# Kernel optimization log

Measured on AMD Instinct MI355X. Metric: run time of the kernel, lower is better.

## Reference

```python
import jax, jax.numpy as jnp
import numpy as np

WINDOW = 512
OVERLAP = 64
STRIDE = WINDOW - OVERLAP  # 448
HEADS = 12
HEAD_DIM = 3072 // HEADS  # 256
SCALE = 1.0 / np.sqrt(HEAD_DIM)


def setup_inputs() -> dict:
    key = jax.random.key(0)
    ks = jax.random.split(key, 9)
    B, S, H = 1, 8192, 3072
    w = 0.02  # weight init scale
    return {
        "hidden_states": jax.random.normal(ks[0], (B, S, H), jnp.float32),
        "Wq": jax.random.normal(ks[1], (H, H), jnp.float32) * w,
        "bq": jnp.zeros((H,), jnp.float32),
        "Wk": jax.random.normal(ks[2], (H, H), jnp.float32) * w,
        "bk": jnp.zeros((H,), jnp.float32),
        "Wv": jax.random.normal(ks[3], (H, H), jnp.float32) * w,
        "bv": jnp.zeros((H,), jnp.float32),
        "Wo": jax.random.normal(ks[4], (H, H), jnp.float32) * w,
        "bo": jnp.zeros((H,), jnp.float32),
    }


def reference(hidden_states, Wq, bq, Wk, bk, Wv, bv, Wo, bo):
    B, S, H = hidden_states.shape
    n_win = -(-S // STRIDE)  # ceil: windows start at 0, STRIDE, 2*STRIDE, ... < S
    starts = np.arange(n_win) * STRIDE                      # static
    idx = starts[:, None] + np.arange(WINDOW)[None, :]      # [n_win, W]
    valid = jnp.asarray(idx < S)                            # [n_win, W] bool
    idx_c = np.minimum(idx, S - 1)                          # clamp for gather

    # Gather overlapping windows: [B, n_win, W, H] (redundant QKV on overlap, as in original)
    win = hidden_states[:, idx_c]

    def proj(Wm, bm):
        y = jnp.einsum('bnwh,oh->bnwo', win, Wm) + bm
        return y.reshape(B, n_win, WINDOW, HEADS, HEAD_DIM)

    q = proj(Wq, bq)
    k = proj(Wk, bk)
    v = proj(Wv, bv)

    scores = jnp.einsum('bnqhd,bnkhd->bnhqk', q, k) * SCALE  # [B,n_win,heads,W,W]
    # Padded (out-of-range) key positions of the short last window must not attend
    scores = jnp.where(valid[None, :, None, None, :], scores, -1e9)
    attn = jax.nn.softmax(scores, axis=-1)
    ctx = jnp.einsum('bnhqk,bnkhd->bnqhd', attn, v)
    ctx = ctx.reshape(B, n_win, WINDOW, H)
    out_w = jnp.einsum('bnwh,oh->bnwo', ctx, Wo) + bo        # [B,n_win,W,H]

    # zero padded query rows, then overlap-add + average
    out_w = out_w * valid[None, :, :, None].astype(out_w.dtype)
    flat_idx = jnp.asarray(idx_c.reshape(-1))                # [n_win*W]
    output = jnp.zeros((B, S, H), out_w.dtype).at[:, flat_idx].add(
        out_w.reshape(B, -1, H))
    counts = jnp.zeros((S,), out_w.dtype).at[flat_idx].add(
        valid.reshape(-1).astype(out_w.dtype))
    return output / jnp.maximum(counts, 1.0)[None, :, None]
```

## Files before the change

kernel.cpp:

```cpp
#include <hip/hip_runtime.h>
#include <hip/hip_bf16.h>
#include <stdint.h>

#define SEQ   8192
#define HDIM  3072
#define NWIN  19
#define WINL  512
#define STR   448
#define NHEAD 12
#define DHEAD 256
#define QKVN  9216
#define ATTN_SCALE 0.0625f

typedef unsigned short u16;
typedef __bf16 bf16x8 __attribute__((ext_vector_type(8)));
typedef float  f32x4  __attribute__((ext_vector_type(4)));
typedef unsigned short us8 __attribute__((ext_vector_type(8)));

__device__ __forceinline__ u16 f2b(float x) {
  return __builtin_bit_cast(u16, __float2bfloat16(x));
}
__device__ __forceinline__ float b2f(u16 u) {
  return __builtin_bit_cast(float, (unsigned int)(u) << 16);
}
__device__ __forceinline__ void gload_lds16(const void* g, void* l) {
  __builtin_amdgcn_global_load_lds(
      (const __attribute__((address_space(1))) void*)g,
      (__attribute__((address_space(3))) void*)l, 16, 0, 0);
}

__global__ __launch_bounds__(256) void cvt_f32_bf16(const float* __restrict__ src,
                                                    u16* __restrict__ dst, int n8) {
  int i = blockIdx.x * 256 + threadIdx.x;
  if (i >= n8) return;
  const float4* s4 = (const float4*)src;
  float4 a = s4[2 * i], b = s4[2 * i + 1];
  us8 o;
  o[0] = f2b(a.x); o[1] = f2b(a.y); o[2] = f2b(a.z); o[3] = f2b(a.w);
  o[4] = f2b(b.x); o[5] = f2b(b.y); o[6] = f2b(b.z); o[7] = f2b(b.w);
  *((us8*)dst + i) = o;
}

__global__ __launch_bounds__(256) void biascat(const float* __restrict__ bq,
                                               const float* __restrict__ bk,
                                               const float* __restrict__ bv,
                                               float* __restrict__ dst) {
  int i = blockIdx.x * 256 + threadIdx.x;
  if (i >= QKVN) return;
  dst[i] = (i < HDIM) ? bq[i] : ((i < 2 * HDIM) ? bk[i - HDIM] : bv[i - 2 * HDIM]);
}

template <bool BF16OUT>
__global__ __launch_bounds__(512, 2) void gemm256(const u16* __restrict__ A,
                                                  const u16* __restrict__ B,
                                                  const float* __restrict__ bias,
                                                  float* __restrict__ outF,
                                                  u16* __restrict__ outB,
                                                  int N, int K) {
  __shared__ __align__(16) u16 As[2][2][128][64];
  __shared__ __align__(16) u16 Bs[2][2][128][64];
  const int tid = threadIdx.x;
  const int w = tid >> 6, l = tid & 63;
  const int wm = w >> 2, wn = w & 3;
  const int fr = l & 15, g = l >> 4;
  const int xcd = blockIdx.x & 7, loc = blockIdx.x >> 3;
  const int bn = loc >> 2, bm = xcd * 4 + (loc & 3);

  const int srow = tid >> 3;
  const int lc = (tid & 7) ^ ((tid >> 3) & 7);
  const u16* sA0 = A + (size_t)(bm * 256 + srow) * K + lc * 8;
  const u16* sA1 = sA0 + (size_t)64 * K;
  const u16* sB0 = B + (size_t)(bn * 256 + srow) * K + lc * 8;
  const u16* sB1 = sB0 + (size_t)64 * K;
  const size_t hiK = (size_t)128 * K;
  const int t16 = tid * 16;
  char* Aw = (char*)As;
  char* Bw = (char*)Bs;

  int rbA[4], rbB[2], ck[2];
#pragma unroll
  for (int i = 0; i < 4; ++i) rbA[i] = (i * 32 + wm * 16 + fr) * 128;
  rbB[0] = (wn * 16 + fr) * 128;
  rbB[1] = (64 + wn * 16 + fr) * 128;
  ck[0] = ((g) ^ (fr & 7)) * 16;
  ck[1] = ((4 + g) ^ (fr & 7)) * 16;

  f32x4 acc[8][4];
#pragma unroll
  for (int i = 0; i < 8; ++i)
#pragma unroll
    for (int j = 0; j < 4; ++j) acc[i][j] = (f32x4){0.f, 0.f, 0.f, 0.f};

  gload_lds16(sA0, Aw + t16); gload_lds16(sA1, Aw + 8192 + t16);
  gload_lds16(sB0, Bw + t16); gload_lds16(sB1, Bw + 8192 + t16);
  gload_lds16(sB0 + hiK, Bw + 16384 + t16); gload_lds16(sB1 + hiK, Bw + 16384 + 8192 + t16);
  gload_lds16(sA0 + hiK, Aw + 16384 + t16); gload_lds16(sA1 + hiK, Aw + 16384 + 8192 + t16);
  sA0 += 64; sA1 += 64; sB0 += 64; sB1 += 64;
  asm volatile("s_waitcnt vmcnt(4)" ::: "memory");
  __builtin_amdgcn_s_barrier();
  __builtin_amdgcn_sched_barrier(0);

  const int NT = K >> 6;
  for (int T = 0; T < NT; ++T) {
    const int cur = T & 1, pp = (T + 1) & 1;
    const bool ds = (T + 1 < NT);
    const bool last = (T == NT - 1);
    const char* ah = (const char*)As + cur * 32768;
    const char* bh = (const char*)Bs + cur * 32768;
    char* apw = Aw + pp * 32768;
    char* bpw = Bw + pp * 32768;
    bf16x8 af[4][2], bf[4][2];

#pragma unroll
    for (int mi = 0; mi < 4; ++mi)
#pragma unroll
      for (int kk = 0; kk < 2; ++kk)
        af[mi][kk] = *(const bf16x8*)(ah + rbA[mi] + ck[kk]);
#pragma unroll
    for (int ni = 0; ni < 2; ++ni)
#pragma unroll
      for (int kk = 0; kk < 2; ++kk)
        bf[ni][kk] = *(const bf16x8*)(bh + rbB[ni] + ck[kk]);
    if (ds) { gload_lds16(sA0, apw + t16); gload_lds16(sA1, apw + 8192 + t16); }
    __builtin_amdgcn_s_barrier();
    asm volatile("s_waitcnt lgkmcnt(0)" ::: "memory");
    __builtin_amdgcn_s_setprio(1);
#pragma unroll
    for (int kk = 0; kk < 2; ++kk)
#pragma unroll
      for (int mi = 0; mi < 4; ++mi)
#pragma unroll
        for (int ni = 0; ni < 2; ++ni)
          acc[mi][ni] = __builtin_amdgcn_mfma_f32_16x16x32_bf16(af[mi][kk], bf[ni][kk], acc[mi][ni], 0, 0, 0);
    __builtin_amdgcn_s_setprio(0);
    if (last) asm volatile("s_waitcnt vmcnt(2)" ::: "memory");
    else      asm volatile("s_waitcnt vmcnt(4)" ::: "memory");
    __builtin_amdgcn_s_barrier();

#pragma unroll
    for (int ni = 2; ni < 4; ++ni)
#pragma unroll
      for (int kk = 0; kk < 2; ++kk)
        bf[ni][kk] = *(const bf16x8*)(bh + 16384 + rbB[ni - 2] + ck[kk]);
    if (ds) { gload_lds16(sB0, bpw + t16); gload_lds16(sB1, bpw + 8192 + t16); }
    __builtin_amdgcn_s_barrier();
    asm volatile("s_waitcnt lgkmcnt(0)" ::: "memory");
    __builtin_amdgcn_s_setprio(1);
#pragma unroll
    for (int kk = 0; kk < 2; ++kk)
#pragma unroll
      for (int mi = 0; mi < 4; ++mi)
#pragma unroll
        for (int ni = 2; ni < 4; ++ni)
          acc[mi][ni] = __builtin_amdgcn_mfma_f32_16x16x32_bf16(af[mi][kk], bf[ni][kk], acc[mi][ni], 0, 0, 0);
    __builtin_amdgcn_s_setprio(0);
    if (last) asm volatile("s_waitcnt vmcnt(0)" ::: "memory");
    else      asm volatile("s_waitcnt vmcnt(4)" ::: "memory");
    __builtin_amdgcn_s_barrier();

#pragma unroll
    for (int mi = 0; mi < 4; ++mi)
#pragma unroll
      for (int kk = 0; kk < 2; ++kk)
        af[mi][kk] = *(const bf16x8*)(ah + 16384 + rbA[mi] + ck[kk]);
    if (ds) { gload_lds16(sB0 + hiK, bpw + 16384 + t16); gload_lds16(sB1 + hiK, bpw + 16384 + 8192 + t16); }
    __builtin_amdgcn_s_barrier();
    asm volatile("s_waitcnt lgkmcnt(0)" ::: "memory");
    __builtin_amdgcn_s_setprio(1);
#pragma unroll
    for (int kk = 0; kk < 2; ++kk)
#pragma unroll
      for (int mi = 0; mi < 4; ++mi)
#pragma unroll
        for (int ni = 0; ni < 2; ++ni)
          acc[mi + 4][ni] = __builtin_amdgcn_mfma_f32_16x16x32_bf16(af[mi][kk], bf[ni][kk], acc[mi + 4][ni], 0, 0, 0);
    __builtin_amdgcn_s_setprio(0);
    __builtin_amdgcn_s_barrier();

    if (ds) { gload_lds16(sA0 + hiK, apw + 16384 + t16); gload_lds16(sA1 + hiK, apw + 16384 + 8192 + t16); }
    __builtin_amdgcn_s_barrier();
    __builtin_amdgcn_s_setprio(1);
#pragma unroll
    for (int kk = 0; kk < 2; ++kk)
#pragma unroll
      for (int mi = 0; mi < 4; ++mi)
#pragma unroll
        for (int ni = 2; ni < 4; ++ni)
          acc[mi + 4][ni] = __builtin_amdgcn_mfma_f32_16x16x32_bf16(af[mi][kk], bf[ni][kk], acc[mi + 4][ni], 0, 0, 0);
    __builtin_amdgcn_s_setprio(0);
    if (!last) asm volatile("s_waitcnt vmcnt(4)" ::: "memory");
    __builtin_amdgcn_s_barrier();
    if (ds) { sA0 += 64; sA1 += 64; sB0 += 64; sB1 += 64; }
    __builtin_amdgcn_sched_barrier(0);
  }

#pragma unroll
  for (int ni = 0; ni < 4; ++ni) {
    const int c = bn * 256 + ni * 64 + wn * 16 + fr;
    const float bvv = bias ? bias[c] : 0.0f;
#pragma unroll
    for (int mi = 0; mi < 8; ++mi) {
      const int r0 = bm * 256 + mi * 32 + wm * 16 + g * 4;
#pragma unroll
      for (int jj = 0; jj < 4; ++jj) {
        float v = acc[mi][ni][jj] + bvv;
        if (BF16OUT) outB[(size_t)(r0 + jj) * N + c] = f2b(v);
        else         outF[(size_t)(r0 + jj) * N + c] = v;
      }
    }
  }
}

__global__ __launch_bounds__(256) void vtrans(const u16* __restrict__ QKV,
                                              u16* __restrict__ Vt) {
  __shared__ u16 t[64][72];
  const int tid = threadIdx.x;
  const int s0 = blockIdx.x * 64, c0 = blockIdx.y * 64;
  {
    const int r2 = tid >> 3, cc = (tid & 7) * 8;
#pragma unroll
    for (int p = 0; p < 2; ++p) {
      const int row = r2 + p * 32;
      u16 tmp[8];
      *(uint4*)tmp = *(const uint4*)(QKV + (size_t)(s0 + row) * QKVN + 2 * HDIM + c0 + cc);
#pragma unroll
      for (int j = 0; j < 8; ++j) t[row][cc + j] = tmp[j];
    }
  }
  __syncthreads();
  {
    const int cr2 = tid >> 3, sc = tid & 7;
#pragma unroll
    for (int p = 0; p < 2; ++p) {
      const int c = cr2 + p * 32;
      u16 tmp[8];
#pragma unroll
      for (int j = 0; j < 8; ++j) tmp[j] = t[sc * 8 + j][c];
      *(uint4*)(Vt + (size_t)(c0 + c) * SEQ + s0 + sc * 8) = *(uint4*)tmp;
    }
  }
}

__global__ __launch_bounds__(256, 2) void attn_kernel(const u16* __restrict__ QKV,
                                                      const u16* __restrict__ Vt,
                                                      u16* __restrict__ ctxw) {
  __shared__ __align__(16) u16 Ks[64 * 256];
  __shared__ __align__(16) u16 Vts[256 * 64];
  __shared__ __align__(16) u16 Ps[4][16 * 64];
  const int qb = blockIdx.x, h = blockIdx.y, n = blockIdx.z;
  const int tid = threadIdx.x, w = tid >> 6, l = tid & 63;
  const int g = l >> 4, fr = l & 15;
  const int s0 = n * STR;

  bf16x8 qf[8];
  {
    int sq = s0 + qb * 64 + w * 16 + fr;
    if (sq > SEQ - 1) sq = SEQ - 1;
    const u16* qbase = QKV + (size_t)sq * QKVN + h * DHEAD + g * 8;
#pragma unroll
    for (int dc = 0; dc < 8; ++dc) qf[dc] = *(const bf16x8*)(qbase + dc * 32);
  }
  f32x4 ctx[16];
#pragma unroll
  for (int dn = 0; dn < 16; ++dn) ctx[dn] = (f32x4){0.f, 0.f, 0.f, 0.f};
  float mrow[4] = {-3e38f, -3e38f, -3e38f, -3e38f};
  float lrow[4] = {0.f, 0.f, 0.f, 0.f};

  const int kr_in = l >> 5;
  const int kcp = l & 31;
  const int vr_in = l >> 3;
  const int vcp = l & 7;

  for (int kt = 0; kt < 8; ++kt) {
    const int sb = s0 + kt * 64;
#pragma unroll
    for (int i = 0; i < 8; ++i) {
      const int c = i * 4 + w;
      {
        const int krow = c * 2 + kr_in;
        const int cl = kcp ^ (krow & 31);
        int sk = sb + krow;
        if (sk > SEQ - 1) sk = SEQ - 1;
        gload_lds16(QKV + (size_t)sk * QKVN + HDIM + h * DHEAD + cl * 8, (char*)Ks + c * 1024);
      }
      {
        const int d = c * 8 + vr_in;
        const int cl = vcp ^ (d & 7);
        int sv = sb + cl * 8;
        if (sv > SEQ - 8) sv = SEQ - 8;
        gload_lds16(Vt + (size_t)(h * DHEAD + d) * SEQ + sv, (char*)Vts + c * 1024);
      }
    }
    __syncthreads();

    f32x4 sacc[4];
#pragma unroll
    for (int kn = 0; kn < 4; ++kn) sacc[kn] = (f32x4){0.f, 0.f, 0.f, 0.f};
#pragma unroll
    for (int kn = 0; kn < 4; ++kn) {
      const int krow = kn * 16 + fr;
      const char* krp = (const char*)Ks + krow * 512;
      const int rx = krow & 31;
#pragma unroll
      for (int dc = 0; dc < 8; ++dc) {
        bf16x8 kf = *(const bf16x8*)(krp + (((dc * 4 + g) ^ rx) << 4));
        sacc[kn] = __builtin_amdgcn_mfma_f32_16x16x32_bf16(qf[dc], kf, sacc[kn], 0, 0, 0);
      }
    }
    float mt[4];
#pragma unroll
    for (int kn = 0; kn < 4; ++kn) {
      const bool valid = (sb + kn * 16 + fr) < SEQ;
#pragma unroll
      for (int r = 0; r < 4; ++r) {
        float v = valid ? sacc[kn][r] * ATTN_SCALE : -1e9f;
        sacc[kn][r] = v;
        mt[r] = (kn == 0) ? v : fmaxf(mt[r], v);
      }
    }
#pragma unroll
    for (int r = 0; r < 4; ++r) {
#pragma unroll
      for (int off = 1; off < 16; off <<= 1)
        mt[r] = fmaxf(mt[r], __shfl_xor(mt[r], off, 64));
    }
    float corr[4];
#pragma unroll
    for (int r = 0; r < 4; ++r) {
      float mnew = fmaxf(mrow[r], mt[r]);
      corr[r] = __expf(mrow[r] - mnew);
      mrow[r] = mnew;
    }
    float psum[4] = {0.f, 0.f, 0.f, 0.f};
    char* pw = (char*)&Ps[w][0];
#pragma unroll
    for (int kn = 0; kn < 4; ++kn) {
#pragma unroll
      for (int r = 0; r < 4; ++r) {
        float p = __expf(sacc[kn][r] - mrow[r]);
        psum[r] += p;
        const int q = g * 4 + r;
        *(u16*)(pw + q * 128 + ((2 * (kn * 16 + fr)) ^ ((q & 7) << 4))) = f2b(p);
      }
    }
#pragma unroll
    for (int r = 0; r < 4; ++r) {
#pragma unroll
      for (int off = 1; off < 16; off <<= 1)
        psum[r] += __shfl_xor(psum[r], off, 64);
      lrow[r] = lrow[r] * corr[r] + psum[r];
    }
#pragma unroll
    for (int dn = 0; dn < 16; ++dn)
#pragma unroll
      for (int r = 0; r < 4; ++r) ctx[dn][r] *= corr[r];
    __syncthreads();

    bf16x8 pf[2];
#pragma unroll
    for (int kc = 0; kc < 2; ++kc)
      pf[kc] = *(const bf16x8*)(pw + fr * 128 + ((kc * 64 + g * 16) ^ ((fr & 7) << 4)));
#pragma unroll
    for (int dn = 0; dn < 16; ++dn) {
      const int d = dn * 16 + fr;
      const char* vrp = (const char*)Vts + d * 128;
      const int dx = d & 7;
#pragma unroll
      for (int kc = 0; kc < 2; ++kc) {
        bf16x8 vf = *(const bf16x8*)(vrp + (((kc * 4 + g) ^ dx) << 4));
        ctx[dn] = __builtin_amdgcn_mfma_f32_16x16x32_bf16(pf[kc], vf, ctx[dn], 0, 0, 0);
      }
    }
    __syncthreads();
  }
  float inv[4];
#pragma unroll
  for (int r = 0; r < 4; ++r) inv[r] = 1.0f / lrow[r];
  const int qrow0 = qb * 64 + w * 16 + g * 4;
#pragma unroll
  for (int dn = 0; dn < 16; ++dn) {
#pragma unroll
    for (int r = 0; r < 4; ++r) {
      ctxw[(size_t)(n * WINL + qrow0 + r) * HDIM + h * DHEAD + dn * 16 + fr] =
          f2b(ctx[dn][r] * inv[r]);
    }
  }
}

__global__ __launch_bounds__(256) void combine_kernel(const u16* __restrict__ ctxw,
                                                      u16* __restrict__ ctx_avg) {
  int idx = blockIdx.x * 256 + threadIdx.x;
  if (idx >= SEQ * (HDIM / 8)) return;
  const int s = idx / (HDIM / 8);
  const int cc = (idx % (HDIM / 8)) * 8;
  const int w1 = s / STR;
  const int off1 = s - w1 * STR;
  us8 a = *(const us8*)(ctxw + (size_t)(w1 * WINL + off1) * HDIM + cc);
  if (w1 >= 1 && off1 < (WINL - STR)) {
    us8 b = *(const us8*)(ctxw + (size_t)((w1 - 1) * WINL + off1 + STR) * HDIM + cc);
#pragma unroll
    for (int j = 0; j < 8; ++j) a[j] = f2b(0.5f * (b2f(a[j]) + b2f(b[j])));
  }
  *(us8*)(ctx_avg + (size_t)s * HDIM + cc) = a;
}

__global__ void ws_marker(float* out, float v) { out[0] = v; }

extern "C" void kernel_launch(void* const* d_in, const int* in_sizes, int n_in,
                              void* d_out, int out_size, void* d_ws, size_t ws_size,
                              hipStream_t stream) {
  const float* X  = (const float*)d_in[0];
  const float* Wq = (const float*)d_in[1];
  const float* bq = (const float*)d_in[2];
  const float* Wk = (const float*)d_in[3];
  const float* bk = (const float*)d_in[4];
  const float* Wv = (const float*)d_in[5];
  const float* bv = (const float*)d_in[6];
  const float* Wo = (const float*)d_in[7];
  const float* bo = (const float*)d_in[8];
  float* out = (float*)d_out;

  const size_t OFF_XB   = 0;
  const size_t OFF_WQKV = 50331648;
  const size_t OFF_WO   = 106954752;
  const size_t OFF_QKV  = 125829120;
  const size_t OFF_VT   = 276824064;
  const size_t OFF_BIAS = 327155712;
  const size_t WS_NEED  = 327192576;
  if (ws_size < WS_NEED) {
    hipMemsetAsync(d_out, 0, (size_t)out_size * 4, stream);
    ws_marker<<<1, 1, 0, stream>>>(out, (float)(ws_size / 1048576));
    return;
  }
  char* ws = (char*)d_ws;
  u16* Xb      = (u16*)(ws + OFF_XB);
  u16* Wqkvb   = (u16*)(ws + OFF_WQKV);
  u16* Wob     = (u16*)(ws + OFF_WO);
  u16* QKV     = (u16*)(ws + OFF_QKV);
  u16* Vt      = (u16*)(ws + OFF_VT);
  float* biasQ = (float*)(ws + OFF_BIAS);
  u16* ctxw    = (u16*)d_out;
  u16* ctx_avg = Xb;

  cvt_f32_bf16<<<12288, 256, 0, stream>>>(X, Xb, SEQ * HDIM / 8);
  cvt_f32_bf16<<<4608, 256, 0, stream>>>(Wq, Wqkvb, HDIM * HDIM / 8);
  cvt_f32_bf16<<<4608, 256, 0, stream>>>(Wk, Wqkvb + (size_t)HDIM * HDIM, HDIM * HDIM / 8);
  cvt_f32_bf16<<<4608, 256, 0, stream>>>(Wv, Wqkvb + (size_t)2 * HDIM * HDIM, HDIM * HDIM / 8);
  cvt_f32_bf16<<<4608, 256, 0, stream>>>(Wo, Wob, HDIM * HDIM / 8);
  biascat<<<36, 256, 0, stream>>>(bq, bk, bv, biasQ);

  gemm256<true><<<dim3((SEQ / 256) * (QKVN / 256)), 512, 0, stream>>>(
      Xb, Wqkvb, biasQ, nullptr, QKV, QKVN, HDIM);

  vtrans<<<dim3(SEQ / 64, HDIM / 64), 256, 0, stream>>>(QKV, Vt);

  attn_kernel<<<dim3(8, NHEAD, NWIN), 256, 0, stream>>>(QKV, Vt, ctxw);

  combine_kernel<<<12288, 256, 0, stream>>>(ctxw, ctx_avg);

  gemm256<false><<<dim3((SEQ / 256) * (HDIM / 256)), 512, 0, stream>>>(
      ctx_avg, Wob, bo, out, nullptr, HDIM, HDIM);
}
```

Before: 858.8 us.

## Restructure GEMM main loop to one barrier per K-tile with staged LDS reads

Rewrites the double-buffered bf16 GEMM inner loop. It replaces four barrier-separated phases, each with partial vmcnt waits, with a single phase per K-tile. That phase issues all next-tile global-to-LDS loads early, interleaves LDS fragment reads with MFMA groups using graded lgkmcnt waits, and synchronises once at the end with vmcnt(0). The goal is to cut barrier count and waiting, and to let LDS reads overlap MFMA. In exchange it keeps more fragment registers live and waits for every global load before the next tile.

```diff
diff --git a/kernel.cpp b/kernel.cpp
--- a/kernel.cpp
+++ b/kernel.cpp
@@ -28,6 +28,7 @@
       (const __attribute__((address_space(1))) void*)g,
       (__attribute__((address_space(3))) void*)l, 16, 0, 0);
 }
+#define SB0() __builtin_amdgcn_sched_barrier(0)
 
 __global__ __launch_bounds__(256) void cvt_f32_bf16(const float* __restrict__ src,
                                                     u16* __restrict__ dst, int n8) {
@@ -96,34 +97,81 @@
   gload_lds16(sB0 + hiK, Bw + 16384 + t16); gload_lds16(sB1 + hiK, Bw + 16384 + 8192 + t16);
   gload_lds16(sA0 + hiK, Aw + 16384 + t16); gload_lds16(sA1 + hiK, Aw + 16384 + 8192 + t16);
   sA0 += 64; sA1 += 64; sB0 += 64; sB1 += 64;
-  asm volatile("s_waitcnt vmcnt(4)" ::: "memory");
+  asm volatile("s_waitcnt vmcnt(0)" ::: "memory");
   __builtin_amdgcn_s_barrier();
-  __builtin_amdgcn_sched_barrier(0);
+  SB0();
 
   const int NT = K >> 6;
   for (int T = 0; T < NT; ++T) {
     const int cur = T & 1, pp = (T + 1) & 1;
     const bool ds = (T + 1 < NT);
-    const bool last = (T == NT - 1);
     const char* ah = (const char*)As + cur * 32768;
     const char* bh = (const char*)Bs + cur * 32768;
     char* apw = Aw + pp * 32768;
     char* bpw = Bw + pp * 32768;
-    bf16x8 af[4][2], bf[4][2];
-
+    bf16x8 afL[4][2], afH[4][2], bfL[2][2], bfH[2][2];
+
+#pragma unroll
+    for (int mi = 0; mi < 4; ++mi) afL[mi][0] = *(const bf16x8*)(ah + rbA[mi] + ck[0]);
+#pragma unroll
+    for (int ni = 0; ni < 2; ++ni) bfL[ni][0] = *(const bf16x8*)(bh + rbB[ni] + ck[0]);
+    SB0();
+    if (ds) {
+      gload_lds16(sA0, apw + t16); gload_lds16(sA1, apw + 8192 + t16);
+      gload_lds16(sB0, bpw + t16); gload_lds16(sB1, bpw + 8192 + t16);
+    }
+#pragma unroll
+    for (int mi = 0; mi < 4; ++mi) afL[mi][1] = *(const bf16x8*)(ah + rbA[mi] + ck[1]);
+#pragma unroll
+    for (int ni = 0; ni < 2; ++ni) bfL[ni][1] = *(const bf16x8*)(bh + rbB[ni] + ck[1]);
+    SB0();
+#pragma unroll
+    for (int ni = 0; ni < 2; ++ni)
+#pragma unroll
+      for (int kk = 0; kk < 2; ++kk)
+        bfH[ni][kk] = *(const bf16x8*)(bh + 16384 + rbB[ni] + ck[kk]);
+    SB0();
+    asm volatile("s_waitcnt lgkmcnt(10)" ::: "memory");
+    SB0();
+    __builtin_amdgcn_s_setprio(1);
 #pragma unroll
     for (int mi = 0; mi < 4; ++mi)
 #pragma unroll
+      for (int ni = 0; ni < 2; ++ni)
+        acc[mi][ni] = __builtin_amdgcn_mfma_f32_16x16x32_bf16(afL[mi][0], bfL[ni][0], acc[mi][ni], 0, 0, 0);
+    __builtin_amdgcn_s_setprio(0);
+    asm volatile("s_waitcnt lgkmcnt(4)" ::: "memory");
+    SB0();
+    __builtin_amdgcn_s_setprio(1);
+#pragma unroll
+    for (int mi = 0; mi < 4; ++mi)
+#pragma unroll
+      for (int ni = 0; ni < 2; ++ni)
+        acc[mi][ni] = __builtin_amdgcn_mfma_f32_16x16x32_bf16(afL[mi][1], bfL[ni][1], acc[mi][ni], 0, 0, 0);
+    __builtin_amdgcn_s_setprio(0);
+#pragma unroll
+    for (int mi = 0; mi < 4; ++mi)
+#pragma unroll
       for (int kk = 0; kk < 2; ++kk)
-        af[mi][kk] = *(const bf16x8*)(ah + rbA[mi] + ck[kk]);
-#pragma unroll
-    for (int ni = 0; ni < 2; ++ni)
-#pragma unroll
-      for (int kk = 0; kk < 2; ++kk)
-        bf[ni][kk] = *(const bf16x8*)(bh + rbB[ni] + ck[kk]);
-    if (ds) { gload_lds16(sA0, apw + t16); gload_lds16(sA1, apw + 8192 + t16); }
-    __builtin_amdgcn_s_barrier();
+        afH[mi][kk] = *(const bf16x8*)(ah + 16384 + rbA[mi] + ck[kk]);
+    SB0();
+    if (ds) {
+      gload_lds16(sB0 + hiK, bpw + 16384 + t16); gload_lds16(sB1 + hiK, bpw + 16384 + 8192 + t16);
+      gload_lds16(sA0 + hiK, apw + 16384 + t16); gload_lds16(sA1 + hiK, apw + 16384 + 8192 + t16);
+    }
+    asm volatile("s_waitcnt lgkmcnt(8)" ::: "memory");
+    SB0();
+    __builtin_amdgcn_s_setprio(1);
+#pragma unroll
+    for (int kk = 0; kk < 2; ++kk)
+#pragma unroll
+      for (int mi = 0; mi < 4; ++mi)
+#pragma unroll
+        for (int ni = 0; ni < 2; ++ni)
+          acc[mi][ni + 2] = __builtin_amdgcn_mfma_f32_16x16x32_bf16(afL[mi][kk], bfH[ni][kk], acc[mi][ni + 2], 0, 0, 0);
+    __builtin_amdgcn_s_setprio(0);
     asm volatile("s_waitcnt lgkmcnt(0)" ::: "memory");
+    SB0();
     __builtin_amdgcn_s_setprio(1);
 #pragma unroll
     for (int kk = 0; kk < 2; ++kk)
@@ -131,67 +179,21 @@
       for (int mi = 0; mi < 4; ++mi)
 #pragma unroll
         for (int ni = 0; ni < 2; ++ni)
-          acc[mi][ni] = __builtin_amdgcn_mfma_f32_16x16x32_bf16(af[mi][kk], bf[ni][kk], acc[mi][ni], 0, 0, 0);
+          acc[mi + 4][ni] = __builtin_amdgcn_mfma_f32_16x16x32_bf16(afH[mi][kk], bfL[ni][kk], acc[mi + 4][ni], 0, 0, 0);
+#pragma unroll
+    for (int kk = 0; kk < 2; ++kk)
+#pragma unroll
+      for (int mi = 0; mi < 4; ++mi)
+#pragma unroll
+        for (int ni = 0; ni < 2; ++ni)
+          acc[mi + 4][ni + 2] = __builtin_amdgcn_mfma_f32_16x16x32_bf16(afH[mi][kk], bfH[ni][kk], acc[mi + 4][ni + 2], 0, 0, 0);
     __builtin_amdgcn_s_setprio(0);
-    if (last) asm volatile("s_waitcnt vmcnt(2)" ::: "memory");
-    else      asm volatile("s_waitcnt vmcnt(4)" ::: "memory");
-    __builtin_amdgcn_s_barrier();
-
-#pragma unroll
-    for (int ni = 2; ni < 4; ++ni)
-#pragma unroll
-      for (int kk = 0; kk < 2; ++kk)
-        bf[ni][kk] = *(const bf16x8*)(bh + 16384 + rbB[ni - 2] + ck[kk]);
-    if (ds) { gload_lds16(sB0, bpw + t16); gload_lds16(sB1, bpw + 8192 + t16); }
-    __builtin_amdgcn_s_barrier();
-    asm volatile("s_waitcnt lgkmcnt(0)" ::: "memory");
-    __builtin_amdgcn_s_setprio(1);
-#pragma unroll
-    for (int kk = 0; kk < 2; ++kk)
-#pragma unroll
-      for (int mi = 0; mi < 4; ++mi)
-#pragma unroll
-        for (int ni = 2; ni < 4; ++ni)
-          acc[mi][ni] = __builtin_amdgcn_mfma_f32_16x16x32_bf16(af[mi][kk], bf[ni][kk], acc[mi][ni], 0, 0, 0);
-    __builtin_amdgcn_s_setprio(0);
-    if (last) asm volatile("s_waitcnt vmcnt(0)" ::: "memory");
-    else      asm volatile("s_waitcnt vmcnt(4)" ::: "memory");
-    __builtin_amdgcn_s_barrier();
-
-#pragma unroll
-    for (int mi = 0; mi < 4; ++mi)
-#pragma unroll
-      for (int kk = 0; kk < 2; ++kk)
-        af[mi][kk] = *(const bf16x8*)(ah + 16384 + rbA[mi] + ck[kk]);
-    if (ds) { gload_lds16(sB0 + hiK, bpw + 16384 + t16); gload_lds16(sB1 + hiK, bpw + 16384 + 8192 + t16); }
-    __builtin_amdgcn_s_barrier();
-    asm volatile("s_waitcnt lgkmcnt(0)" ::: "memory");
-    __builtin_amdgcn_s_setprio(1);
-#pragma unroll
-    for (int kk = 0; kk < 2; ++kk)
-#pragma unroll
-      for (int mi = 0; mi < 4; ++mi)
-#pragma unroll
-        for (int ni = 0; ni < 2; ++ni)
-          acc[mi + 4][ni] = __builtin_amdgcn_mfma_f32_16x16x32_bf16(af[mi][kk], bf[ni][kk], acc[mi + 4][ni], 0, 0, 0);
-    __builtin_amdgcn_s_setprio(0);
-    __builtin_amdgcn_s_barrier();
-
-    if (ds) { gload_lds16(sA0 + hiK, apw + 16384 + t16); gload_lds16(sA1 + hiK, apw + 16384 + 8192 + t16); }
-    __builtin_amdgcn_s_barrier();
-    __builtin_amdgcn_s_setprio(1);
-#pragma unroll
-    for (int kk = 0; kk < 2; ++kk)
-#pragma unroll
-      for (int mi = 0; mi < 4; ++mi)
-#pragma unroll
-        for (int ni = 2; ni < 4; ++ni)
-          acc[mi + 4][ni] = __builtin_amdgcn_mfma_f32_16x16x32_bf16(af[mi][kk], bf[ni][kk], acc[mi + 4][ni], 0, 0, 0);
-    __builtin_amdgcn_s_setprio(0);
-    if (!last) asm volatile("s_waitcnt vmcnt(4)" ::: "memory");
-    __builtin_amdgcn_s_barrier();
-    if (ds) { sA0 += 64; sA1 += 64; sB0 += 64; sB1 += 64; }
-    __builtin_amdgcn_sched_barrier(0);
+    if (ds) {
+      asm volatile("s_waitcnt vmcnt(0)" ::: "memory");
+      __builtin_amdgcn_s_barrier();
+      sA0 += 64; sA1 += 64; sB0 += 64; sB1 += 64;
+    }
+    SB0();
   }
 
 #pragma unroll
```

Result: slower. 931.3 us (+8.4%).

## Unroll GEMM main loop by two K-tiles and reschedule global-to-LDS prefetches

Applied to the files above, without the earlier changes.

The bf16 MFMA GEMM main loop now handles two 64-wide K tiles per iteration. The prologue loads tile 0 and part of tile 1, and the remaining quarter-tile global-to-LDS copies are spread across the MFMA phases of both halves through a small staging lambda. Waitcnt and barrier placement is rewritten to match, including a partial lgkmcnt wait before the first barrier. The aim is deeper prefetch so global-load latency hides better behind MFMA work. The risk is that the hand-tuned vmcnt counts no longer match the outstanding loads, and the extra unrolling raises register pressure.

```diff
diff --git a/kernel.cpp b/kernel.cpp
--- a/kernel.cpp
+++ b/kernel.cpp
@@ -28,6 +28,7 @@
       (const __attribute__((address_space(1))) void*)g,
       (__attribute__((address_space(3))) void*)l, 16, 0, 0);
 }
+#define SB0() __builtin_amdgcn_sched_barrier(0)
 
 __global__ __launch_bounds__(256) void cvt_f32_bf16(const float* __restrict__ src,
                                                     u16* __restrict__ dst, int n8) {
@@ -68,14 +69,18 @@
 
   const int srow = tid >> 3;
   const int lc = (tid & 7) ^ ((tid >> 3) & 7);
-  const u16* sA0 = A + (size_t)(bm * 256 + srow) * K + lc * 8;
-  const u16* sA1 = sA0 + (size_t)64 * K;
-  const u16* sB0 = B + (size_t)(bn * 256 + srow) * K + lc * 8;
-  const u16* sB1 = sB0 + (size_t)64 * K;
-  const size_t hiK = (size_t)128 * K;
+  const u16* sAb = A + (size_t)(bm * 256 + srow) * K + lc * 8;
+  const u16* sBb = B + (size_t)(bn * 256 + srow) * K + lc * 8;
   const int t16 = tid * 16;
   char* Aw = (char*)As;
   char* Bw = (char*)Bs;
+
+  auto stage = [&](const u16* base, char* lds, int tile, int half) {
+    const u16* s = base + (size_t)half * 128 * K + (size_t)tile * 64;
+    char* d = lds + (tile & 1) * 32768 + half * 16384 + t16;
+    gload_lds16(s, d);
+    gload_lds16(s + (size_t)64 * K, d + 8192);
+  };
 
   int rbA[4], rbB[2], ck[2];
 #pragma unroll
@@ -91,107 +96,116 @@
 #pragma unroll
     for (int j = 0; j < 4; ++j) acc[i][j] = (f32x4){0.f, 0.f, 0.f, 0.f};
 
-  gload_lds16(sA0, Aw + t16); gload_lds16(sA1, Aw + 8192 + t16);
-  gload_lds16(sB0, Bw + t16); gload_lds16(sB1, Bw + 8192 + t16);
-  gload_lds16(sB0 + hiK, Bw + 16384 + t16); gload_lds16(sB1 + hiK, Bw + 16384 + 8192 + t16);
-  gload_lds16(sA0 + hiK, Aw + 16384 + t16); gload_lds16(sA1 + hiK, Aw + 16384 + 8192 + t16);
-  sA0 += 64; sA1 += 64; sB0 += 64; sB1 += 64;
+  stage(sAb, Aw, 0, 0); stage(sAb, Aw, 0, 1);
+  stage(sBb, Bw, 0, 0); stage(sBb, Bw, 0, 1);
+  stage(sAb, Aw, 1, 0); stage(sBb, Bw, 1, 0);
   asm volatile("s_waitcnt vmcnt(4)" ::: "memory");
   __builtin_amdgcn_s_barrier();
-  __builtin_amdgcn_sched_barrier(0);
-
-  const int NT = K >> 6;
-  for (int T = 0; T < NT; ++T) {
-    const int cur = T & 1, pp = (T + 1) & 1;
-    const bool ds = (T + 1 < NT);
-    const bool last = (T == NT - 1);
-    const char* ah = (const char*)As + cur * 32768;
-    const char* bh = (const char*)Bs + cur * 32768;
-    char* apw = Aw + pp * 32768;
-    char* bpw = Bw + pp * 32768;
-    bf16x8 af[4][2], bf[4][2];
-
-#pragma unroll
-    for (int mi = 0; mi < 4; ++mi)
+  SB0();
+
+  const int NJ = K >> 7;
+  for (int j = 0; j < NJ; ++j) {
+    const int t0 = 2 * j;
+    const bool st23 = (j + 1 < NJ);
+    const bool lastj = (j == NJ - 1);
+    bf16x8 af[4][2], bfL[2][2], bfH[2][2];
+
+#pragma unroll
+    for (int half = 0; half < 2; ++half) {
+      const char* ah = (const char*)As + half * 32768;
+      const char* bh = (const char*)Bs + half * 32768;
+
+#pragma unroll
+      for (int mi = 0; mi < 4; ++mi)
+#pragma unroll
+        for (int kk = 0; kk < 2; ++kk)
+          af[mi][kk] = *(const bf16x8*)(ah + rbA[mi] + ck[kk]);
+#pragma unroll
+      for (int ni = 0; ni < 2; ++ni)
+#pragma unroll
+        for (int kk = 0; kk < 2; ++kk)
+          bfL[ni][kk] = *(const bf16x8*)(bh + rbB[ni] + ck[kk]);
+      if (half == 0) stage(sBb, Bw, t0 + 1, 1);
+      else if (st23) stage(sAb, Aw, t0 + 3, 0);
+      if (half == 1) {  }
+      asm volatile("s_waitcnt lgkmcnt(8)" ::: "memory");
+      __builtin_amdgcn_s_barrier();
+      asm volatile("s_waitcnt lgkmcnt(0)" ::: "memory");
+      SB0();
+      __builtin_amdgcn_s_setprio(1);
 #pragma unroll
       for (int kk = 0; kk < 2; ++kk)
-        af[mi][kk] = *(const bf16x8*)(ah + rbA[mi] + ck[kk]);
-#pragma unroll
-    for (int ni = 0; ni < 2; ++ni)
+#pragma unroll
+        for (int mi = 0; mi < 4; ++mi)
+#pragma unroll
+          for (int ni = 0; ni < 2; ++ni)
+            acc[mi][ni] = __builtin_amdgcn_mfma_f32_16x16x32_bf16(af[mi][kk], bfL[ni][kk], acc[mi][ni], 0, 0, 0);
+      __builtin_amdgcn_s_setprio(0);
+      __builtin_amdgcn_s_barrier();
+
+#pragma unroll
+      for (int ni = 0; ni < 2; ++ni)
+#pragma unroll
+        for (int kk = 0; kk < 2; ++kk)
+          bfH[ni][kk] = *(const bf16x8*)(bh + 16384 + rbB[ni] + ck[kk]);
+      if (half == 0) stage(sAb, Aw, t0 + 1, 1);
+      else if (st23) stage(sAb, Aw, t0 + 2, 1);
+      __builtin_amdgcn_s_barrier();
+      asm volatile("s_waitcnt lgkmcnt(0)" ::: "memory");
+      SB0();
+      __builtin_amdgcn_s_setprio(1);
 #pragma unroll
       for (int kk = 0; kk < 2; ++kk)
-        bf[ni][kk] = *(const bf16x8*)(bh + rbB[ni] + ck[kk]);
-    if (ds) { gload_lds16(sA0, apw + t16); gload_lds16(sA1, apw + 8192 + t16); }
-    __builtin_amdgcn_s_barrier();
-    asm volatile("s_waitcnt lgkmcnt(0)" ::: "memory");
-    __builtin_amdgcn_s_setprio(1);
-#pragma unroll
-    for (int kk = 0; kk < 2; ++kk)
+#pragma unroll
+        for (int mi = 0; mi < 4; ++mi)
+#pragma unroll
+          for (int ni = 0; ni < 2; ++ni)
+            acc[mi][ni + 2] = __builtin_amdgcn_mfma_f32_16x16x32_bf16(af[mi][kk], bfH[ni][kk], acc[mi][ni + 2], 0, 0, 0);
+      __builtin_amdgcn_s_setprio(0);
+      __builtin_amdgcn_s_barrier();
+
 #pragma unroll
       for (int mi = 0; mi < 4; ++mi)
 #pragma unroll
-        for (int ni = 0; ni < 2; ++ni)
-          acc[mi][ni] = __builtin_amdgcn_mfma_f32_16x16x32_bf16(af[mi][kk], bf[ni][kk], acc[mi][ni], 0, 0, 0);
-    __builtin_amdgcn_s_setprio(0);
-    if (last) asm volatile("s_waitcnt vmcnt(2)" ::: "memory");
-    else      asm volatile("s_waitcnt vmcnt(4)" ::: "memory");
-    __builtin_amdgcn_s_barrier();
-
-#pragma unroll
-    for (int ni = 2; ni < 4; ++ni)
+        for (int kk = 0; kk < 2; ++kk)
+          af[mi][kk] = *(const bf16x8*)(ah + 16384 + rbA[mi] + ck[kk]);
+      if (half == 0) { if (st23) stage(sAb, Aw, t0 + 2, 0); }
+      else           { if (st23) stage(sBb, Bw, t0 + 3, 0); }
+      __builtin_amdgcn_s_barrier();
+      asm volatile("s_waitcnt lgkmcnt(0)" ::: "memory");
+      SB0();
+      __builtin_amdgcn_s_setprio(1);
 #pragma unroll
       for (int kk = 0; kk < 2; ++kk)
-        bf[ni][kk] = *(const bf16x8*)(bh + 16384 + rbB[ni - 2] + ck[kk]);
-    if (ds) { gload_lds16(sB0, bpw + t16); gload_lds16(sB1, bpw + 8192 + t16); }
-    __builtin_amdgcn_s_barrier();
-    asm volatile("s_waitcnt lgkmcnt(0)" ::: "memory");
-    __builtin_amdgcn_s_setprio(1);
-#pragma unroll
-    for (int kk = 0; kk < 2; ++kk)
-#pragma unroll
-      for (int mi = 0; mi < 4; ++mi)
-#pragma unroll
-        for (int ni = 2; ni < 4; ++ni)
-          acc[mi][ni] = __builtin_amdgcn_mfma_f32_16x16x32_bf16(af[mi][kk], bf[ni][kk], acc[mi][ni], 0, 0, 0);
-    __builtin_amdgcn_s_setprio(0);
-    if (last) asm volatile("s_waitcnt vmcnt(0)" ::: "memory");
-    else      asm volatile("s_waitcnt vmcnt(4)" ::: "memory");
-    __builtin_amdgcn_s_barrier();
-
-#pragma unroll
-    for (int mi = 0; mi < 4; ++mi)
+#pragma unroll
+        for (int mi = 0; mi < 4; ++mi)
+#pragma unroll
+          for (int ni = 0; ni < 2; ++ni)
+            acc[mi + 4][ni] = __builtin_amdgcn_mfma_f32_16x16x32_bf16(af[mi][kk], bfL[ni][kk], acc[mi + 4][ni], 0, 0, 0);
+      __builtin_amdgcn_s_setprio(0);
+      __builtin_amdgcn_s_barrier();
+
+      if (half == 0) { if (st23) stage(sBb, Bw, t0 + 2, 0); }
+      __builtin_amdgcn_s_barrier();
+      __builtin_amdgcn_s_setprio(1);
 #pragma unroll
       for (int kk = 0; kk < 2; ++kk)
-        af[mi][kk] = *(const bf16x8*)(ah + 16384 + rbA[mi] + ck[kk]);
-    if (ds) { gload_lds16(sB0 + hiK, bpw + 16384 + t16); gload_lds16(sB1 + hiK, bpw + 16384 + 8192 + t16); }
-    __builtin_amdgcn_s_barrier();
-    asm volatile("s_waitcnt lgkmcnt(0)" ::: "memory");
-    __builtin_amdgcn_s_setprio(1);
-#pragma unroll
-    for (int kk = 0; kk < 2; ++kk)
-#pragma unroll
-      for (int mi = 0; mi < 4; ++mi)
-#pragma unroll
-        for (int ni = 0; ni < 2; ++ni)
-          acc[mi + 4][ni] = __builtin_amdgcn_mfma_f32_16x16x32_bf16(af[mi][kk], bf[ni][kk], acc[mi + 4][ni], 0, 0, 0);
-    __builtin_amdgcn_s_setprio(0);
-    __builtin_amdgcn_s_barrier();
-
-    if (ds) { gload_lds16(sA0 + hiK, apw + 16384 + t16); gload_lds16(sA1 + hiK, apw + 16384 + 8192 + t16); }
-    __builtin_amdgcn_s_barrier();
-    __builtin_amdgcn_s_setprio(1);
-#pragma unroll
-    for (int kk = 0; kk < 2; ++kk)
-#pragma unroll
-      for (int mi = 0; mi < 4; ++mi)
-#pragma unroll
-        for (int ni = 2; ni < 4; ++ni)
-          acc[mi + 4][ni] = __builtin_amdgcn_mfma_f32_16x16x32_bf16(af[mi][kk], bf[ni][kk], acc[mi + 4][ni], 0, 0, 0);
-    __builtin_amdgcn_s_setprio(0);
-    if (!last) asm volatile("s_waitcnt vmcnt(4)" ::: "memory");
-    __builtin_amdgcn_s_barrier();
-    if (ds) { sA0 += 64; sA1 += 64; sB0 += 64; sB1 += 64; }
-    __builtin_amdgcn_sched_barrier(0);
+#pragma unroll
+        for (int mi = 0; mi < 4; ++mi)
+#pragma unroll
+          for (int ni = 0; ni < 2; ++ni)
+            acc[mi + 4][ni + 2] = __builtin_amdgcn_mfma_f32_16x16x32_bf16(af[mi][kk], bfH[ni][kk], acc[mi + 4][ni + 2], 0, 0, 0);
+      __builtin_amdgcn_s_setprio(0);
+      if (half == 0) {
+        if (lastj) asm volatile("s_waitcnt vmcnt(0)" ::: "memory");
+        else       asm volatile("s_waitcnt vmcnt(4)" ::: "memory");
+      } else if (!lastj) {
+        asm volatile("s_waitcnt vmcnt(4)" ::: "memory");
+      }
+      __builtin_amdgcn_s_barrier();
+      SB0();
+    }
+    if (st23) stage(sBb, Bw, t0 + 2, 1);
   }
 
 #pragma unroll
```

After: 923.7 us. 7.6% more time.

## Fuse V transpose into QKV GEMM epilogue and double-buffer attention K/V tiles

Applied to the files above, without the earlier changes.

The QKV GEMM epilogue now also writes the V columns in transposed layout, so the separate vtrans kernel launch and its extra pass over V are gone. The attention kernel switches to 32-key tiles held in two LDS buffers and prefetches the next tile while the current one is computed. This removes one barrier per iteration and shrinks the P buffer, at the cost of twice as many loop trips and strided 8-byte transposed stores in the GEMM epilogue. sched_barrier hints are also added before the MFMA blocks of the GEMM.

```diff
diff --git a/kernel.cpp b/kernel.cpp
--- a/kernel.cpp
+++ b/kernel.cpp
@@ -10,6 +10,7 @@
 #define NHEAD 12
 #define DHEAD 256
 #define QKVN  9216
+#define KVB   32
 #define ATTN_SCALE 0.0625f
 
 typedef unsigned short u16;
@@ -56,6 +57,7 @@
                                                   const float* __restrict__ bias,
                                                   float* __restrict__ outF,
                                                   u16* __restrict__ outB,
+                                                  u16* __restrict__ vtOut,
                                                   int N, int K) {
   __shared__ __align__(16) u16 As[2][2][128][64];
   __shared__ __align__(16) u16 Bs[2][2][128][64];
@@ -124,6 +126,7 @@
     if (ds) { gload_lds16(sA0, apw + t16); gload_lds16(sA1, apw + 8192 + t16); }
     __builtin_amdgcn_s_barrier();
     asm volatile("s_waitcnt lgkmcnt(0)" ::: "memory");
+    __builtin_amdgcn_sched_barrier(0);
     __builtin_amdgcn_s_setprio(1);
 #pragma unroll
     for (int kk = 0; kk < 2; ++kk)
@@ -145,6 +148,7 @@
     if (ds) { gload_lds16(sB0, bpw + t16); gload_lds16(sB1, bpw + 8192 + t16); }
     __builtin_amdgcn_s_barrier();
     asm volatile("s_waitcnt lgkmcnt(0)" ::: "memory");
+    __builtin_amdgcn_sched_barrier(0);
     __builtin_amdgcn_s_setprio(1);
 #pragma unroll
     for (int kk = 0; kk < 2; ++kk)
@@ -166,6 +170,7 @@
     if (ds) { gload_lds16(sB0 + hiK, bpw + 16384 + t16); gload_lds16(sB1 + hiK, bpw + 16384 + 8192 + t16); }
     __builtin_amdgcn_s_barrier();
     asm volatile("s_waitcnt lgkmcnt(0)" ::: "memory");
+    __builtin_amdgcn_sched_barrier(0);
     __builtin_amdgcn_s_setprio(1);
 #pragma unroll
     for (int kk = 0; kk < 2; ++kk)
@@ -198,45 +203,18 @@
   for (int ni = 0; ni < 4; ++ni) {
     const int c = bn * 256 + ni * 64 + wn * 16 + fr;
     const float bvv = bias ? bias[c] : 0.0f;
+    const bool wv = BF16OUT && (vtOut != nullptr) && (c >= 2 * HDIM);
 #pragma unroll
     for (int mi = 0; mi < 8; ++mi) {
       const int r0 = bm * 256 + mi * 32 + wm * 16 + g * 4;
+      u16 t4[4];
 #pragma unroll
       for (int jj = 0; jj < 4; ++jj) {
         float v = acc[mi][ni][jj] + bvv;
-        if (BF16OUT) outB[(size_t)(r0 + jj) * N + c] = f2b(v);
+        if (BF16OUT) { u16 b_ = f2b(v); outB[(size_t)(r0 + jj) * N + c] = b_; t4[jj] = b_; }
         else         outF[(size_t)(r0 + jj) * N + c] = v;
       }
-    }
-  }
-}
-
-__global__ __launch_bounds__(256) void vtrans(const u16* __restrict__ QKV,
-                                              u16* __restrict__ Vt) {
-  __shared__ u16 t[64][72];
-  const int tid = threadIdx.x;
-  const int s0 = blockIdx.x * 64, c0 = blockIdx.y * 64;
-  {
-    const int r2 = tid >> 3, cc = (tid & 7) * 8;
-#pragma unroll
-    for (int p = 0; p < 2; ++p) {
-      const int row = r2 + p * 32;
-      u16 tmp[8];
-      *(uint4*)tmp = *(const uint4*)(QKV + (size_t)(s0 + row) * QKVN + 2 * HDIM + c0 + cc);
-#pragma unroll
-      for (int j = 0; j < 8; ++j) t[row][cc + j] = tmp[j];
-    }
-  }
-  __syncthreads();
-  {
-    const int cr2 = tid >> 3, sc = tid & 7;
-#pragma unroll
-    for (int p = 0; p < 2; ++p) {
-      const int c = cr2 + p * 32;
-      u16 tmp[8];
-#pragma unroll
-      for (int j = 0; j < 8; ++j) tmp[j] = t[sc * 8 + j][c];
-      *(uint4*)(Vt + (size_t)(c0 + c) * SEQ + s0 + sc * 8) = *(uint4*)tmp;
+      if (wv) *(uint2*)(vtOut + (size_t)(c - 2 * HDIM) * SEQ + r0) = *(const uint2*)t4;
     }
   }
 }
@@ -244,9 +222,9 @@
 __global__ __launch_bounds__(256, 2) void attn_kernel(const u16* __restrict__ QKV,
                                                       const u16* __restrict__ Vt,
                                                       u16* __restrict__ ctxw) {
-  __shared__ __align__(16) u16 Ks[64 * 256];
-  __shared__ __align__(16) u16 Vts[256 * 64];
-  __shared__ __align__(16) u16 Ps[4][16 * 64];
+  __shared__ __align__(16) u16 Ks[2][KVB * 256];
+  __shared__ __align__(16) u16 Vs[2][256 * KVB];
+  __shared__ __align__(16) u16 Ps[4][16 * KVB];
   const int qb = blockIdx.x, h = blockIdx.y, n = blockIdx.z;
   const int tid = threadIdx.x, w = tid >> 6, l = tid & 63;
   const int g = l >> 4, fr = l & 15;
@@ -266,50 +244,59 @@
   float mrow[4] = {-3e38f, -3e38f, -3e38f, -3e38f};
   float lrow[4] = {0.f, 0.f, 0.f, 0.f};
 
-  const int kr_in = l >> 5;
-  const int kcp = l & 31;
-  const int vr_in = l >> 3;
-  const int vcp = l & 7;
-
-  for (int kt = 0; kt < 8; ++kt) {
-    const int sb = s0 + kt * 64;
-#pragma unroll
-    for (int i = 0; i < 8; ++i) {
+  auto stage = [&](int kt) {
+    const int sb = s0 + kt * KVB;
+#pragma unroll
+    for (int i = 0; i < 4; ++i) {
       const int c = i * 4 + w;
       {
-        const int krow = c * 2 + kr_in;
-        const int cl = kcp ^ (krow & 31);
+        const int krow = c * 2 + (l >> 5);
+        const int cl = (l & 31) ^ krow;
         int sk = sb + krow;
         if (sk > SEQ - 1) sk = SEQ - 1;
-        gload_lds16(QKV + (size_t)sk * QKVN + HDIM + h * DHEAD + cl * 8, (char*)Ks + c * 1024);
+        gload_lds16(QKV + (size_t)sk * QKVN + HDIM + h * DHEAD + cl * 8,
+                    (char*)&Ks[kt & 1][0] + c * 1024);
       }
       {
-        const int d = c * 8 + vr_in;
-        const int cl = vcp ^ (d & 7);
+        const int d = c * 16 + (l >> 2);
+        const int cl = (l & 3) ^ (d & 3) ^ ((d >> 2) & 3);
         int sv = sb + cl * 8;
         if (sv > SEQ - 8) sv = SEQ - 8;
-        gload_lds16(Vt + (size_t)(h * DHEAD + d) * SEQ + sv, (char*)Vts + c * 1024);
-      }
-    }
-    __syncthreads();
-
-    f32x4 sacc[4];
-#pragma unroll
-    for (int kn = 0; kn < 4; ++kn) sacc[kn] = (f32x4){0.f, 0.f, 0.f, 0.f};
-#pragma unroll
-    for (int kn = 0; kn < 4; ++kn) {
+        gload_lds16(Vt + (size_t)(h * DHEAD + d) * SEQ + sv,
+                    (char*)&Vs[kt & 1][0] + c * 1024);
+      }
+    }
+  };
+
+  stage(0);
+  const int mv = (fr & 3) ^ ((fr >> 2) & 3);
+  char* pw = (char*)&Ps[w][0];
+
+  for (int kt = 0; kt < 16; ++kt) {
+    asm volatile("s_waitcnt vmcnt(0)" ::: "memory");
+    __builtin_amdgcn_s_barrier();
+    __builtin_amdgcn_sched_barrier(0);
+    if (kt + 1 < 16) stage(kt + 1);
+    const char* kb = (const char*)&Ks[kt & 1][0];
+    const char* vb = (const char*)&Vs[kt & 1][0];
+    const int sb = s0 + kt * KVB;
+
+    f32x4 sacc[2];
+#pragma unroll
+    for (int kn = 0; kn < 2; ++kn) sacc[kn] = (f32x4){0.f, 0.f, 0.f, 0.f};
+#pragma unroll
+    for (int kn = 0; kn < 2; ++kn) {
       const int krow = kn * 16 + fr;
-      const char* krp = (const char*)Ks + krow * 512;
-      const int rx = krow & 31;
+      const char* krp = kb + krow * 512;
 #pragma unroll
       for (int dc = 0; dc < 8; ++dc) {
-        bf16x8 kf = *(const bf16x8*)(krp + (((dc * 4 + g) ^ rx) << 4));
+        bf16x8 kf = *(const bf16x8*)(krp + (((dc * 4 + g) ^ krow) << 4));
         sacc[kn] = __builtin_amdgcn_mfma_f32_16x16x32_bf16(qf[dc], kf, sacc[kn], 0, 0, 0);
       }
     }
     float mt[4];
 #pragma unroll
-    for (int kn = 0; kn < 4; ++kn) {
+    for (int kn = 0; kn < 2; ++kn) {
       const bool valid = (sb + kn * 16 + fr) < SEQ;
 #pragma unroll
       for (int r = 0; r < 4; ++r) {
@@ -332,15 +319,15 @@
       mrow[r] = mnew;
     }
     float psum[4] = {0.f, 0.f, 0.f, 0.f};
-    char* pw = (char*)&Ps[w][0];
-#pragma unroll
-    for (int kn = 0; kn < 4; ++kn) {
+#pragma unroll
+    for (int kn = 0; kn < 2; ++kn) {
 #pragma unroll
       for (int r = 0; r < 4; ++r) {
         float p = __expf(sacc[kn][r] - mrow[r]);
         psum[r] += p;
         const int q = g * 4 + r;
-        *(u16*)(pw + q * 128 + ((2 * (kn * 16 + fr)) ^ ((q & 7) << 4))) = f2b(p);
+        const int kv = kn * 16 + fr;
+        *(u16*)(pw + q * 64 + ((((kv >> 3) ^ r ^ g) << 4) | ((2 * kv) & 15))) = f2b(p);
       }
     }
 #pragma unroll
@@ -354,24 +341,14 @@
     for (int dn = 0; dn < 16; ++dn)
 #pragma unroll
       for (int r = 0; r < 4; ++r) ctx[dn][r] *= corr[r];
-    __syncthreads();
-
-    bf16x8 pf[2];
-#pragma unroll
-    for (int kc = 0; kc < 2; ++kc)
-      pf[kc] = *(const bf16x8*)(pw + fr * 128 + ((kc * 64 + g * 16) ^ ((fr & 7) << 4)));
+
+    bf16x8 pf = *(const bf16x8*)(pw + fr * 64 + ((g ^ mv) << 4));
 #pragma unroll
     for (int dn = 0; dn < 16; ++dn) {
       const int d = dn * 16 + fr;
-      const char* vrp = (const char*)Vts + d * 128;
-      const int dx = d & 7;
-#pragma unroll
-      for (int kc = 0; kc < 2; ++kc) {
-        bf16x8 vf = *(const bf16x8*)(vrp + (((kc * 4 + g) ^ dx) << 4));
-        ctx[dn] = __builtin_amdgcn_mfma_f32_16x16x32_bf16(pf[kc], vf, ctx[dn], 0, 0, 0);
-      }
-    }
-    __syncthreads();
+      bf16x8 vf = *(const bf16x8*)(vb + d * 64 + ((g ^ mv) << 4));
+      ctx[dn] = __builtin_amdgcn_mfma_f32_16x16x32_bf16(pf, vf, ctx[dn], 0, 0, 0);
+    }
   }
   float inv[4];
 #pragma unroll
@@ -450,14 +427,12 @@
   biascat<<<36, 256, 0, stream>>>(bq, bk, bv, biasQ);
 
   gemm256<true><<<dim3((SEQ / 256) * (QKVN / 256)), 512, 0, stream>>>(
-      Xb, Wqkvb, biasQ, nullptr, QKV, QKVN, HDIM);
-
-  vtrans<<<dim3(SEQ / 64, HDIM / 64), 256, 0, stream>>>(QKV, Vt);
+      Xb, Wqkvb, biasQ, nullptr, QKV, Vt, QKVN, HDIM);
 
   attn_kernel<<<dim3(8, NHEAD, NWIN), 256, 0, stream>>>(QKV, Vt, ctxw);
 
   combine_kernel<<<12288, 256, 0, stream>>>(ctxw, ctx_avg);
 
   gemm256<false><<<dim3((SEQ / 256) * (HDIM / 256)), 512, 0, stream>>>(
-      ctx_avg, Wob, bo, out, nullptr, HDIM, HDIM);
-}
+      ctx_avg, Wob, bo, out, nullptr, nullptr, HDIM, HDIM);
+}
```

Measured after the change: 903.2 us. +5.2%, slower.
